# Kernel tuning notes

Measured on AMD Instinct MI355X. Metric: run time of the kernel, lower is better.

The kernel has to match this reference:

```python
import jax, jax.numpy as jnp
import numpy as np

M, L, D, V = 4096, 15, 1024, 32  # moves, word_max, in_sz, vocab_sz


def setup_inputs() -> dict:
    key = jax.random.key(0)
    ks = jax.random.split(key, 9)
    s = 0.02
    return {
        "tokens": jax.random.randint(ks[0], (M, L), 0, V),
        "letter_emb": jax.random.normal(ks[1], (V, D), jnp.float32) * s,
        "pos_emb": jax.random.normal(ks[2], (L, D), jnp.float32) * s,
        "Wq": jax.random.normal(ks[3], (D, D), jnp.float32) * s,
        "bq": jax.random.normal(ks[4], (D,), jnp.float32) * s,
        "Wk": jax.random.normal(ks[5], (D, D), jnp.float32) * s,
        "bk": jax.random.normal(ks[6], (D,), jnp.float32) * s,
        "Wv": jax.random.normal(ks[7], (D, D), jnp.float32) * s,
        "bv": jax.random.normal(ks[8], (D,), jnp.float32) * s,
    }


def reference(tokens, letter_emb, pos_emb, Wq, bq, Wk, bk, Wv, bv):
    # WordEncoder, batched across all M moves.
    x = letter_emb[tokens] + pos_emb[None, :, :]          # [M, L, D]
    q = jnp.einsum("mld,ed->mle", x, Wq) + bq             # Linear: x @ W.T + b
    k = jnp.einsum("mld,ed->mle", x, Wk) + bk
    v = jnp.einsum("mld,ed->mle", x, Wv) + bv
    scores = jax.nn.softmax(jnp.einsum("mle,mke->mlk", q, k), axis=-1)  # [M, L, L]
    attn = jnp.einsum("mlk,mke->mle", scores, v)          # [M, L, D]
    word = attn.sum(axis=1)                               # [M, D]
    # enc = word + ordered, where ordered is an identical second evaluation
    # of word_enc on the same word -> enc = 2 * word.
    return 2.0 * word
```

## Files before the change

### kernel.cpp

```cpp
#include <hip/hip_runtime.h>
#include <hip/hip_bf16.h>

#define NMOVES 4096
#define LW     15
#define DIM    1024
#define VOC    32
#define XROW   48
#define KSPL   4
#define GSPL   8
#define PLSZ   (48 * DIM)
#define GPLSZ  (48 * 64)

typedef __attribute__((ext_vector_type(8))) short  short8;
typedef __attribute__((ext_vector_type(4))) float  floatx4;

__device__ __forceinline__ unsigned short f2b(float f) {
  unsigned int x;
  __builtin_memcpy(&x, &f, 4);
  x = x + 0x7FFFu + ((x >> 16) & 1u);
  return (unsigned short)(x >> 16);
}
__device__ __forceinline__ float b2f(unsigned short u) {
  unsigned int x = ((unsigned int)u) << 16;
  float f;
  __builtin_memcpy(&f, &x, 4);
  return f;
}
__device__ __forceinline__ short8 pk8(float4 a, float4 b) {
  short8 r;
  r[0] = (short)f2b(a.x); r[1] = (short)f2b(a.y);
  r[2] = (short)f2b(a.z); r[3] = (short)f2b(a.w);
  r[4] = (short)f2b(b.x); r[5] = (short)f2b(b.y);
  r[6] = (short)f2b(b.z); r[7] = (short)f2b(b.w);
  return r;
}
__device__ __forceinline__ float4 ld4(const float* p) {
  return *reinterpret_cast<const float4*>(p);
}

__global__ __launch_bounds__(256) void proj_ksplit(
    const float* __restrict__ letter, const float* __restrict__ pos,
    const float* __restrict__ Wq, const float* __restrict__ Wk,
    const float* __restrict__ Wv, float* __restrict__ Xp) {
  const int p     = blockIdx.x;
  const int bn0   = blockIdx.y * 64;
  const int z     = blockIdx.z;
  const int kbase = p * 256;
  const float* W = (z == 0) ? Wq : (z == 1) ? Wk : Wv;
  float*       O = Xp + (size_t)(z * KSPL + p) * PLSZ;

  const int tid  = threadIdx.x;
  const int lane = tid & 63;
  const int wave = tid >> 6;
  const int wr   = wave >> 1;
  const int wc   = wave & 1;
  const int quad = lane >> 4;
  const int l16  = lane & 15;

  const int rA0 = wr * 32 + l16;
  const int rA1 = rA0 + 16;
  const float* a0p = (rA0 < 32) ? letter + (size_t)rA0 * DIM
                   : (rA0 < 47) ? pos + (size_t)(rA0 - 32) * DIM : nullptr;
  const float* a1p = (rA1 < 32) ? letter + (size_t)rA1 * DIM
                   : (rA1 < 47) ? pos + (size_t)(rA1 - 32) * DIM : nullptr;
  const float* b0p = W + (size_t)(bn0 + wc * 32 + l16) * DIM;
  const float* b1p = b0p + (size_t)16 * DIM;

  floatx4 acc[2][2];
#pragma unroll
  for (int i = 0; i < 2; ++i)
#pragma unroll
    for (int j = 0; j < 2; ++j) acc[i][j] = (floatx4){0.f, 0.f, 0.f, 0.f};

  const short8 z8 = (short8){0,0,0,0,0,0,0,0};
#pragma unroll
  for (int kk = 0; kk < 256; kk += 32) {
    const int kc = kbase + kk + quad * 8;
    short8 a0 = a0p ? pk8(ld4(a0p + kc), ld4(a0p + kc + 4)) : z8;
    short8 a1 = a1p ? pk8(ld4(a1p + kc), ld4(a1p + kc + 4)) : z8;
    short8 b0 = pk8(ld4(b0p + kc), ld4(b0p + kc + 4));
    short8 b1 = pk8(ld4(b1p + kc), ld4(b1p + kc + 4));
    acc[0][0] = __builtin_amdgcn_mfma_f32_16x16x32_bf16(a0, b0, acc[0][0], 0, 0, 0);
    acc[0][1] = __builtin_amdgcn_mfma_f32_16x16x32_bf16(a0, b1, acc[0][1], 0, 0, 0);
    acc[1][0] = __builtin_amdgcn_mfma_f32_16x16x32_bf16(a1, b0, acc[1][0], 0, 0, 0);
    acc[1][1] = __builtin_amdgcn_mfma_f32_16x16x32_bf16(a1, b1, acc[1][1], 0, 0, 0);
  }

#pragma unroll
  for (int mi = 0; mi < 2; ++mi) {
#pragma unroll
    for (int ni = 0; ni < 2; ++ni) {
      const int gcol = bn0 + wc * 32 + ni * 16 + l16;
#pragma unroll
      for (int i = 0; i < 4; ++i) {
        const int grow = wr * 32 + mi * 16 + quad * 4 + i;
        if (grow < 47)
          O[(size_t)grow * DIM + gcol] = acc[mi][ni][i];
      }
    }
  }
}

__device__ __forceinline__ short8 gfrag(const float* __restrict__ X4,
                                        const float* __restrict__ bias,
                                        int row, int kc) {
  if (row < 47) {
    const float* r0 = X4 + (size_t)row * DIM + kc;
    float4 s0 = ld4(r0),            s1 = ld4(r0 + 4);
    float4 t0 = ld4(r0 + PLSZ),     t1 = ld4(r0 + PLSZ + 4);
    float4 u0 = ld4(r0 + 2 * PLSZ), u1 = ld4(r0 + 2 * PLSZ + 4);
    float4 v0 = ld4(r0 + 3 * PLSZ), v1 = ld4(r0 + 3 * PLSZ + 4);
    s0.x += t0.x + u0.x + v0.x; s0.y += t0.y + u0.y + v0.y;
    s0.z += t0.z + u0.z + v0.z; s0.w += t0.w + u0.w + v0.w;
    s1.x += t1.x + u1.x + v1.x; s1.y += t1.y + u1.y + v1.y;
    s1.z += t1.z + u1.z + v1.z; s1.w += t1.w + u1.w + v1.w;
    return pk8(s0, s1);
  } else if (row == 47) {
    return pk8(ld4(bias + kc), ld4(bias + kc + 4));
  }
  return (short8){0,0,0,0,0,0,0,0};
}

__global__ __launch_bounds__(256) void gram_vexp(
    const float* __restrict__ Xp,
    const float* __restrict__ bq, const float* __restrict__ bk,
    float* __restrict__ Gp8, unsigned short* __restrict__ XvT) {
  const int bid = blockIdx.x;
  const int tid = threadIdx.x;

  if (bid < GSPL) {
    const int kbase = bid * 128;
    const int lane = tid & 63;
    const int wave = tid >> 6;
    const int wr   = wave >> 1;
    const int wc   = wave & 1;
    const int quad = lane >> 4;
    const int l16  = lane & 15;

    const float* Xq4 = Xp;
    const float* Xk4 = Xp + (size_t)4 * PLSZ;
    const int rA0 = wr * 32 + l16, rA1 = rA0 + 16;
    const int rB0 = wc * 32 + l16, rB1 = rB0 + 16;

    floatx4 acc[2][2];
#pragma unroll
    for (int i = 0; i < 2; ++i)
#pragma unroll
      for (int j = 0; j < 2; ++j) acc[i][j] = (floatx4){0.f, 0.f, 0.f, 0.f};

#pragma unroll
    for (int kk = 0; kk < 128; kk += 32) {
      const int kc = kbase + kk + quad * 8;
      short8 a0 = gfrag(Xq4, bq, rA0, kc);
      short8 a1 = gfrag(Xq4, bq, rA1, kc);
      short8 b0 = gfrag(Xk4, bk, rB0, kc);
      short8 b1 = gfrag(Xk4, bk, rB1, kc);
      acc[0][0] = __builtin_amdgcn_mfma_f32_16x16x32_bf16(a0, b0, acc[0][0], 0, 0, 0);
      acc[0][1] = __builtin_amdgcn_mfma_f32_16x16x32_bf16(a0, b1, acc[0][1], 0, 0, 0);
      acc[1][0] = __builtin_amdgcn_mfma_f32_16x16x32_bf16(a1, b0, acc[1][0], 0, 0, 0);
      acc[1][1] = __builtin_amdgcn_mfma_f32_16x16x32_bf16(a1, b1, acc[1][1], 0, 0, 0);
    }

    float* Gout = Gp8 + (size_t)bid * GPLSZ;
#pragma unroll
    for (int mi = 0; mi < 2; ++mi) {
#pragma unroll
      for (int ni = 0; ni < 2; ++ni) {
        const int gcol = wc * 32 + ni * 16 + l16;
#pragma unroll
        for (int i = 0; i < 4; ++i) {
          const int grow = wr * 32 + mi * 16 + quad * 4 + i;
          if (grow < XROW)
            Gout[(size_t)grow * 64 + gcol] = acc[mi][ni][i];
        }
      }
    }
  } else {
    const int n  = (bid - GSPL) * 64 + (tid & 63);
    const int kg = tid >> 6;
    const float* Xv4 = Xp + (size_t)8 * PLSZ;
#pragma unroll
    for (int s = 0; s < 4; ++s) {
      const int k0 = kg * 4 + s * 16;
      ushort4 o;
      unsigned short* oc = &o.x;
#pragma unroll
      for (int i = 0; i < 4; ++i) {
        const int k = k0 + i;
        float v = 0.f;
        if (k < 47) {
          const size_t off = (size_t)k * DIM + n;
          v = Xv4[off] + Xv4[off + PLSZ] + Xv4[off + 2 * PLSZ] +
              Xv4[off + 3 * PLSZ];
        }
        oc[i] = f2b(v);
      }
      *reinterpret_cast<ushort4*>(XvT + (size_t)n * 64 + k0) = o;
    }
  }
}

__global__ __launch_bounds__(256) void coef_k(
    const void* __restrict__ tokens_raw, const float* __restrict__ Gp8,
    unsigned short* __restrict__ C) {
  __shared__ float Gs[XROW * 65];
  __shared__ float Sm[16][LW][17];
  __shared__ float CL[16][64];
  __shared__ int   tokL[16][16];
  __shared__ int   is64_s;
  const int m0  = blockIdx.x * 16;
  const int tid = threadIdx.x;

  const unsigned int* u32 = (const unsigned int*)tokens_raw;
  if (tid < 64) {
    unsigned int v = u32[2 * tid + 1];
    unsigned long long nz = __ballot(v != 0);
    if (tid == 0) is64_s = (nz == 0ULL) ? 1 : 0;
  }
#pragma unroll
  for (int i = 0; i < 12; ++i) {
    const int idx = i * 256 + tid;
    float s = 0.f;
#pragma unroll
    for (int p = 0; p < GSPL; ++p) s += Gp8[(size_t)p * GPLSZ + idx];
    Gs[(idx >> 6) * 65 + (idx & 63)] = s;
  }
  {
    const int g = tid >> 4, L = tid & 15;
#pragma unroll
    for (int i = 0; i < 4; ++i) CL[g][L * 4 + i] = 0.f;
  }
  __syncthreads();

  if (tid < 16 * LW) {
    const int mv = tid / LW, j = tid - mv * LW;
    int t;
    if (is64_s) t = (int)((const long long*)tokens_raw)[(size_t)(m0 + mv) * LW + j];
    else        t = ((const int*)tokens_raw)[(size_t)(m0 + mv) * LW + j];
    tokL[mv][j] = t;
  }
  __syncthreads();

  const int g = tid >> 4;
  const int L = tid & 15;
  if (L < LW) {
    const int rb0 = tokL[g][L] * 65;
    const int rb1 = (32 + L) * 65;
    const int rb2 = (XROW - 1) * 65;
    float S[LW];
#pragma unroll
    for (int j = 0; j < LW; ++j) {
      const int c0 = tokL[g][j];
      const int c1 = 32 + j;
      S[j] = Gs[rb0 + c0] + Gs[rb1 + c0] + Gs[rb2 + c0]
           + Gs[rb0 + c1] + Gs[rb1 + c1] + Gs[rb2 + c1];
    }
    float mx = S[0];
#pragma unroll
    for (int j = 1; j < LW; ++j) mx = fmaxf(mx, S[j]);
    float sum = 0.f;
#pragma unroll
    for (int j = 0; j < LW; ++j) { S[j] = __expf(S[j] - mx); sum += S[j]; }
    const float inv = 1.0f / sum;
#pragma unroll
    for (int j = 0; j < LW; ++j) Sm[g][L][j] = S[j] * inv;
  }
  __syncthreads();

  if (L < LW) {
    float s = 0.f;
#pragma unroll
    for (int l = 0; l < LW; ++l) s += Sm[g][l][L];
    const float wj = 2.0f * s;
    atomicAdd(&CL[g][tokL[g][L]], wj);
    CL[g][32 + L] = wj;
  }
  __syncthreads();

  float4 cv = *reinterpret_cast<const float4*>(&CL[g][L * 4]);
  ushort4 hi, lo;
  hi.x = f2b(cv.x); hi.y = f2b(cv.y); hi.z = f2b(cv.z); hi.w = f2b(cv.w);
  lo.x = f2b(cv.x - b2f(hi.x)); lo.y = f2b(cv.y - b2f(hi.y));
  lo.z = f2b(cv.z - b2f(hi.z)); lo.w = f2b(cv.w - b2f(hi.w));
  unsigned short* Crow = C + (size_t)(m0 + g) * 128;
  *reinterpret_cast<ushort4*>(Crow + L * 4)      = hi;
  *reinterpret_cast<ushort4*>(Crow + 64 + L * 4) = lo;
}

__global__ __launch_bounds__(256) void out_gemm(
    const unsigned short* __restrict__ C, const unsigned short* __restrict__ XvT,
    const float* __restrict__ bv, float* __restrict__ out) {
  const int bm0 = blockIdx.x * 64;
  const int bn0 = blockIdx.y * 64;
  const int tid  = threadIdx.x;
  const int lane = tid & 63;
  const int wave = tid >> 6;
  const int wr   = wave >> 1;
  const int wc   = wave & 1;
  const int quad = lane >> 4;
  const int l16  = lane & 15;

  const unsigned short* A0 = C + (size_t)(bm0 + wr * 32 + l16) * 128;
  const unsigned short* A1 = A0 + 16 * 128;
  const unsigned short* B0 = XvT + (size_t)(bn0 + wc * 32 + l16) * 64;
  const unsigned short* B1 = B0 + 16 * 64;

  floatx4 acc[2][2];
#pragma unroll
  for (int i = 0; i < 2; ++i)
#pragma unroll
    for (int j = 0; j < 2; ++j) acc[i][j] = (floatx4){0.f, 0.f, 0.f, 0.f};

#pragma unroll
  for (int ks = 0; ks < 64; ks += 32) {
    short8 b0  = *reinterpret_cast<const short8*>(B0 + ks + quad * 8);
    short8 b1  = *reinterpret_cast<const short8*>(B1 + ks + quad * 8);
    short8 a0h = *reinterpret_cast<const short8*>(A0 + ks + quad * 8);
    short8 a1h = *reinterpret_cast<const short8*>(A1 + ks + quad * 8);
    short8 a0l = *reinterpret_cast<const short8*>(A0 + 64 + ks + quad * 8);
    short8 a1l = *reinterpret_cast<const short8*>(A1 + 64 + ks + quad * 8);
    acc[0][0] = __builtin_amdgcn_mfma_f32_16x16x32_bf16(a0h, b0, acc[0][0], 0, 0, 0);
    acc[0][0] = __builtin_amdgcn_mfma_f32_16x16x32_bf16(a0l, b0, acc[0][0], 0, 0, 0);
    acc[0][1] = __builtin_amdgcn_mfma_f32_16x16x32_bf16(a0h, b1, acc[0][1], 0, 0, 0);
    acc[0][1] = __builtin_amdgcn_mfma_f32_16x16x32_bf16(a0l, b1, acc[0][1], 0, 0, 0);
    acc[1][0] = __builtin_amdgcn_mfma_f32_16x16x32_bf16(a1h, b0, acc[1][0], 0, 0, 0);
    acc[1][0] = __builtin_amdgcn_mfma_f32_16x16x32_bf16(a1l, b0, acc[1][0], 0, 0, 0);
    acc[1][1] = __builtin_amdgcn_mfma_f32_16x16x32_bf16(a1h, b1, acc[1][1], 0, 0, 0);
    acc[1][1] = __builtin_amdgcn_mfma_f32_16x16x32_bf16(a1l, b1, acc[1][1], 0, 0, 0);
  }

#pragma unroll
  for (int mi = 0; mi < 2; ++mi) {
#pragma unroll
    for (int ni = 0; ni < 2; ++ni) {
      const int gcol = bn0 + wc * 32 + ni * 16 + l16;
      const float bias30 = 30.0f * bv[gcol];
#pragma unroll
      for (int i = 0; i < 4; ++i) {
        const int grow = bm0 + wr * 32 + mi * 16 + quad * 4 + i;
        out[(size_t)grow * DIM + gcol] = acc[mi][ni][i] + bias30;
      }
    }
  }
}

extern "C" void kernel_launch(void* const* d_in, const int* in_sizes, int n_in,
                              void* d_out, int out_size, void* d_ws, size_t ws_size,
                              hipStream_t stream) {
  const void*  tokens = d_in[0];
  const float* letter = (const float*)d_in[1];
  const float* pos    = (const float*)d_in[2];
  const float* Wq     = (const float*)d_in[3];
  const float* bq     = (const float*)d_in[4];
  const float* Wk     = (const float*)d_in[5];
  const float* bk     = (const float*)d_in[6];
  const float* Wv     = (const float*)d_in[7];
  const float* bv     = (const float*)d_in[8];
  float*       outp   = (float*)d_out;

  char* ws = (char*)d_ws;
  const size_t XP_SZ  = (size_t)12 * PLSZ * 4;
  const size_t GP_SZ  = (size_t)GSPL * GPLSZ * 4;
  const size_t XVT_SZ = (size_t)DIM * 64 * 2;
  float*          Xp  = (float*)(ws);
  float*          Gp  = (float*)(ws + XP_SZ);
  unsigned short* XvT = (unsigned short*)(ws + XP_SZ + GP_SZ);
  unsigned short* Cc  = (unsigned short*)(ws + XP_SZ + GP_SZ + XVT_SZ);

  proj_ksplit<<<dim3(KSPL, 16, 3), 256, 0, stream>>>(letter, pos, Wq, Wk, Wv, Xp);
  gram_vexp<<<GSPL + 16, 256, 0, stream>>>(Xp, bq, bk, Gp, XvT);
  coef_k<<<NMOVES / 16, 256, 0, stream>>>(tokens, Gp, Cc);
  out_gemm<<<dim3(NMOVES / 64, DIM / 64), 256, 0, stream>>>(Cc, XvT, bv, outp);
}
```

Before: 118.7 us.

## Fuse coefficient softmax into output GEMM and atomically reduce Gram partials

```diff
diff --git a/kernel.cpp b/kernel.cpp
--- a/kernel.cpp
+++ b/kernel.cpp
@@ -9,7 +9,6 @@
 #define KSPL   4
 #define GSPL   8
 #define PLSZ   (48 * DIM)
-#define GPLSZ  (48 * 64)
 
 typedef __attribute__((ext_vector_type(8))) short  short8;
 typedef __attribute__((ext_vector_type(4))) float  floatx4;
@@ -41,7 +40,14 @@
 __global__ __launch_bounds__(256) void proj_ksplit(
     const float* __restrict__ letter, const float* __restrict__ pos,
     const float* __restrict__ Wq, const float* __restrict__ Wk,
-    const float* __restrict__ Wv, float* __restrict__ Xp) {
+    const float* __restrict__ Wv, float* __restrict__ Xp,
+    float* __restrict__ G48) {
+  const int tid = threadIdx.x;
+  if (blockIdx.x == 0 && blockIdx.y == 0 && blockIdx.z == 0) {
+#pragma unroll
+    for (int i = 0; i < (XROW * 64) / 256; ++i) G48[i * 256 + tid] = 0.f;
+  }
+
   const int p     = blockIdx.x;
   const int bn0   = blockIdx.y * 64;
   const int z     = blockIdx.z;
@@ -49,7 +55,6 @@
   const float* W = (z == 0) ? Wq : (z == 1) ? Wk : Wv;
   float*       O = Xp + (size_t)(z * KSPL + p) * PLSZ;
 
-  const int tid  = threadIdx.x;
   const int lane = tid & 63;
   const int wave = tid >> 6;
   const int wr   = wave >> 1;
@@ -124,7 +129,7 @@
 __global__ __launch_bounds__(256) void gram_vexp(
     const float* __restrict__ Xp,
     const float* __restrict__ bq, const float* __restrict__ bk,
-    float* __restrict__ Gp8, unsigned short* __restrict__ XvT) {
+    float* __restrict__ G48, unsigned short* __restrict__ XvT) {
   const int bid = blockIdx.x;
   const int tid = threadIdx.x;
 
@@ -161,7 +166,6 @@
       acc[1][1] = __builtin_amdgcn_mfma_f32_16x16x32_bf16(a1, b1, acc[1][1], 0, 0, 0);
     }
 
-    float* Gout = Gp8 + (size_t)bid * GPLSZ;
 #pragma unroll
     for (int mi = 0; mi < 2; ++mi) {
 #pragma unroll
@@ -171,7 +175,7 @@
         for (int i = 0; i < 4; ++i) {
           const int grow = wr * 32 + mi * 16 + quad * 4 + i;
           if (grow < XROW)
-            Gout[(size_t)grow * 64 + gcol] = acc[mi][ni][i];
+            atomicAdd(&G48[(size_t)grow * 64 + gcol], acc[mi][ni][i]);
         }
       }
     }
@@ -200,15 +204,19 @@
   }
 }
 
-__global__ __launch_bounds__(256) void coef_k(
-    const void* __restrict__ tokens_raw, const float* __restrict__ Gp8,
-    unsigned short* __restrict__ C) {
+__global__ __launch_bounds__(256) void attn_gemm(
+    const void* __restrict__ tokens_raw, const float* __restrict__ G48,
+    const unsigned short* __restrict__ XvT, const float* __restrict__ bv,
+    float* __restrict__ out) {
   __shared__ float Gs[XROW * 65];
   __shared__ float Sm[16][LW][17];
   __shared__ float CL[16][64];
+  __shared__ __attribute__((aligned(16))) unsigned short CLh[16 * 72];
+  __shared__ __attribute__((aligned(16))) unsigned short CLl[16 * 72];
   __shared__ int   tokL[16][16];
   __shared__ int   is64_s;
   const int m0  = blockIdx.x * 16;
+  const int cb0 = blockIdx.y * 256;
   const int tid = threadIdx.x;
 
   const unsigned int* u32 = (const unsigned int*)tokens_raw;
@@ -220,10 +228,7 @@
 #pragma unroll
   for (int i = 0; i < 12; ++i) {
     const int idx = i * 256 + tid;
-    float s = 0.f;
-#pragma unroll
-    for (int p = 0; p < GSPL; ++p) s += Gp8[(size_t)p * GPLSZ + idx];
-    Gs[(idx >> 6) * 65 + (idx & 63)] = s;
+    Gs[(idx >> 6) * 65 + (idx & 63)] = G48[idx];
   }
   {
     const int g = tid >> 4, L = tid & 15;
@@ -277,69 +282,47 @@
   }
   __syncthreads();
 
-  float4 cv = *reinterpret_cast<const float4*>(&CL[g][L * 4]);
-  ushort4 hi, lo;
-  hi.x = f2b(cv.x); hi.y = f2b(cv.y); hi.z = f2b(cv.z); hi.w = f2b(cv.w);
-  lo.x = f2b(cv.x - b2f(hi.x)); lo.y = f2b(cv.y - b2f(hi.y));
-  lo.z = f2b(cv.z - b2f(hi.z)); lo.w = f2b(cv.w - b2f(hi.w));
-  unsigned short* Crow = C + (size_t)(m0 + g) * 128;
-  *reinterpret_cast<ushort4*>(Crow + L * 4)      = hi;
-  *reinterpret_cast<ushort4*>(Crow + 64 + L * 4) = lo;
-}
-
-__global__ __launch_bounds__(256) void out_gemm(
-    const unsigned short* __restrict__ C, const unsigned short* __restrict__ XvT,
-    const float* __restrict__ bv, float* __restrict__ out) {
-  const int bm0 = blockIdx.x * 64;
-  const int bn0 = blockIdx.y * 64;
-  const int tid  = threadIdx.x;
+  {
+    float4 cv = *reinterpret_cast<const float4*>(&CL[g][L * 4]);
+    ushort4 hi, lo;
+    hi.x = f2b(cv.x); hi.y = f2b(cv.y); hi.z = f2b(cv.z); hi.w = f2b(cv.w);
+    lo.x = f2b(cv.x - b2f(hi.x)); lo.y = f2b(cv.y - b2f(hi.y));
+    lo.z = f2b(cv.z - b2f(hi.z)); lo.w = f2b(cv.w - b2f(hi.w));
+    *reinterpret_cast<ushort4*>(CLh + g * 72 + L * 4) = hi;
+    *reinterpret_cast<ushort4*>(CLl + g * 72 + L * 4) = lo;
+  }
+  __syncthreads();
+
   const int lane = tid & 63;
   const int wave = tid >> 6;
-  const int wr   = wave >> 1;
-  const int wc   = wave & 1;
   const int quad = lane >> 4;
   const int l16  = lane & 15;
-
-  const unsigned short* A0 = C + (size_t)(bm0 + wr * 32 + l16) * 128;
-  const unsigned short* A1 = A0 + 16 * 128;
-  const unsigned short* B0 = XvT + (size_t)(bn0 + wc * 32 + l16) * 64;
-  const unsigned short* B1 = B0 + 16 * 64;
-
-  floatx4 acc[2][2];
-#pragma unroll
-  for (int i = 0; i < 2; ++i)
-#pragma unroll
-    for (int j = 0; j < 2; ++j) acc[i][j] = (floatx4){0.f, 0.f, 0.f, 0.f};
+  const int colb = cb0 + wave * 64;
+
+  floatx4 acc[4];
+#pragma unroll
+  for (int i = 0; i < 4; ++i) acc[i] = (floatx4){0.f, 0.f, 0.f, 0.f};
 
 #pragma unroll
   for (int ks = 0; ks < 64; ks += 32) {
-    short8 b0  = *reinterpret_cast<const short8*>(B0 + ks + quad * 8);
-    short8 b1  = *reinterpret_cast<const short8*>(B1 + ks + quad * 8);
-    short8 a0h = *reinterpret_cast<const short8*>(A0 + ks + quad * 8);
-    short8 a1h = *reinterpret_cast<const short8*>(A1 + ks + quad * 8);
-    short8 a0l = *reinterpret_cast<const short8*>(A0 + 64 + ks + quad * 8);
-    short8 a1l = *reinterpret_cast<const short8*>(A1 + 64 + ks + quad * 8);
-    acc[0][0] = __builtin_amdgcn_mfma_f32_16x16x32_bf16(a0h, b0, acc[0][0], 0, 0, 0);
-    acc[0][0] = __builtin_amdgcn_mfma_f32_16x16x32_bf16(a0l, b0, acc[0][0], 0, 0, 0);
-    acc[0][1] = __builtin_amdgcn_mfma_f32_16x16x32_bf16(a0h, b1, acc[0][1], 0, 0, 0);
-    acc[0][1] = __builtin_amdgcn_mfma_f32_16x16x32_bf16(a0l, b1, acc[0][1], 0, 0, 0);
-    acc[1][0] = __builtin_amdgcn_mfma_f32_16x16x32_bf16(a1h, b0, acc[1][0], 0, 0, 0);
-    acc[1][0] = __builtin_amdgcn_mfma_f32_16x16x32_bf16(a1l, b0, acc[1][0], 0, 0, 0);
-    acc[1][1] = __builtin_amdgcn_mfma_f32_16x16x32_bf16(a1h, b1, acc[1][1], 0, 0, 0);
-    acc[1][1] = __builtin_amdgcn_mfma_f32_16x16x32_bf16(a1l, b1, acc[1][1], 0, 0, 0);
-  }
-
-#pragma unroll
-  for (int mi = 0; mi < 2; ++mi) {
-#pragma unroll
-    for (int ni = 0; ni < 2; ++ni) {
-      const int gcol = bn0 + wc * 32 + ni * 16 + l16;
-      const float bias30 = 30.0f * bv[gcol];
-#pragma unroll
-      for (int i = 0; i < 4; ++i) {
-        const int grow = bm0 + wr * 32 + mi * 16 + quad * 4 + i;
-        out[(size_t)grow * DIM + gcol] = acc[mi][ni][i] + bias30;
-      }
+    short8 ah = *reinterpret_cast<const short8*>(CLh + l16 * 72 + ks + quad * 8);
+    short8 al = *reinterpret_cast<const short8*>(CLl + l16 * 72 + ks + quad * 8);
+#pragma unroll
+    for (int ni = 0; ni < 4; ++ni) {
+      const unsigned short* B = XvT + (size_t)(colb + ni * 16 + l16) * 64;
+      short8 b = *reinterpret_cast<const short8*>(B + ks + quad * 8);
+      acc[ni] = __builtin_amdgcn_mfma_f32_16x16x32_bf16(ah, b, acc[ni], 0, 0, 0);
+      acc[ni] = __builtin_amdgcn_mfma_f32_16x16x32_bf16(al, b, acc[ni], 0, 0, 0);
+    }
+  }
+
+#pragma unroll
+  for (int ni = 0; ni < 4; ++ni) {
+    const int gcol = colb + ni * 16 + l16;
+    const float bias30 = 30.0f * bv[gcol];
+#pragma unroll
+    for (int i = 0; i < 4; ++i) {
+      out[(size_t)(m0 + quad * 4 + i) * DIM + gcol] = acc[ni][i] + bias30;
     }
   }
 }
@@ -360,15 +343,13 @@
 
   char* ws = (char*)d_ws;
   const size_t XP_SZ  = (size_t)12 * PLSZ * 4;
-  const size_t GP_SZ  = (size_t)GSPL * GPLSZ * 4;
-  const size_t XVT_SZ = (size_t)DIM * 64 * 2;
+  const size_t G_SZ   = (size_t)XROW * 64 * 4;
   float*          Xp  = (float*)(ws);
   float*          Gp  = (float*)(ws + XP_SZ);
-  unsigned short* XvT = (unsigned short*)(ws + XP_SZ + GP_SZ);
-  unsigned short* Cc  = (unsigned short*)(ws + XP_SZ + GP_SZ + XVT_SZ);
-
-  proj_ksplit<<<dim3(KSPL, 16, 3), 256, 0, stream>>>(letter, pos, Wq, Wk, Wv, Xp);
+  unsigned short* XvT = (unsigned short*)(ws + XP_SZ + G_SZ);
+
+  proj_ksplit<<<dim3(KSPL, 16, 3), 256, 0, stream>>>(letter, pos, Wq, Wk, Wv,
+                                                     Xp, Gp);
   gram_vexp<<<GSPL + 16, 256, 0, stream>>>(Xp, bq, bk, Gp, XvT);
-  coef_k<<<NMOVES / 16, 256, 0, stream>>>(tokens, Gp, Cc);
-  out_gemm<<<dim3(NMOVES / 64, DIM / 64), 256, 0, stream>>>(Cc, XvT, bv, outp);
-}
+  attn_gemm<<<dim3(NMOVES / 16, 4), 256, 0, stream>>>(tokens, Gp, XvT, bv, outp);
+}
```

Measured after the change: 113.9 us. 1.04x faster.
